# Optimization experiments

Measured on AMD Instinct MI355X. Metric: run time of the kernel, lower is better.

## Reference

```python
import jax, jax.numpy as jnp
import numpy as np

B, N, E = 16, 1000, 16000        # graphs, nodes/graph, edges/graph
H1, C1 = 8, 128                  # conv1 heads, per-head channels (hidden_size)
EMB, HID = 64, 128               # embed_size, mlp hidden_size


def gat_conv(x, ei, W, att_src, att_dst, bias, heads, concat):
    """PyG GATConv (eval mode, self-loops already in ei). x: [Ntot, Fin]."""
    Ntot = x.shape[0]
    C = W.shape[1] // heads
    h = (x @ W).reshape(Ntot, heads, C)                  # [Ntot, H, C]
    a_src = jnp.einsum('nhc,hc->nh', h, att_src)          # [Ntot, H]
    a_dst = jnp.einsum('nhc,hc->nh', h, att_dst)
    src, dst = ei[0], ei[1]
    alpha = jax.nn.leaky_relu(a_src[src] + a_dst[dst], 0.2)   # [Etot, H]
    # segment softmax over destination nodes (every node has a self loop)
    amax = jax.ops.segment_max(alpha, dst, num_segments=Ntot)
    ea = jnp.exp(alpha - amax[dst])
    denom = jax.ops.segment_sum(ea, dst, num_segments=Ntot)
    alpha = ea / denom[dst]
    msg = h[src] * alpha[:, :, None]                      # [Etot, H, C]
    out = jax.ops.segment_sum(msg, dst, num_segments=Ntot)   # [Ntot, H, C]
    out = out.reshape(Ntot, heads * C) if concat else out.mean(axis=1)
    return out + bias


def setup_inputs():
    key = jax.random.key(0)
    k = jax.random.split(key, 16)
    g = lambda kk, sh: (jax.random.normal(kk, sh, jnp.float32) * 0.1)
    return {
        'actions': jax.random.normal(k[0], (B, N, 2), jnp.float32),
        'node_features': jax.random.normal(k[1], (B, 1, N), jnp.float32),
        'edge_index': jax.random.randint(k[2], (B, 2, E), 0, N, dtype=jnp.int32),
        # conv1: GATConv(3, C1, heads=H1, concat=True)
        'W1': g(k[3], (3, H1 * C1)),
        'att_src1': g(k[4], (H1, C1)),
        'att_dst1': g(k[5], (H1, C1)),
        'b1': g(k[6], (H1 * C1,)),
        # conv2: GATConv(H1*C1, EMB, heads=1, concat=False)
        'W2': g(k[7], (H1 * C1, EMB)),
        'att_src2': g(k[8], (1, EMB)),
        'att_dst2': g(k[9], (1, EMB)),
        'b2': g(k[10], (EMB,)),
        # MLP head
        'mlp_w1': g(k[11], (N * EMB, HID)),
        'mlp_b1': jnp.zeros((HID,), jnp.float32),
        'mlp_w2': g(k[12], (HID, HID)),
        'mlp_b2': jnp.zeros((HID,), jnp.float32),
        'out_w': g(k[13], (HID, N)),
        'out_b': jnp.zeros((N,), jnp.float32),
    }


def reference(actions, node_features, edge_index, W1, att_src1, att_dst1, b1,
              W2, att_src2, att_dst2, b2, mlp_w1, mlp_b1, mlp_w2, mlp_b2,
              out_w, out_b):
    Bn, _, Nn = node_features.shape
    nf = node_features.astype(jnp.float32).squeeze(1)                 # [B, N]
    x = jnp.stack([actions[:, :, 0], actions[:, :, 1], nf], axis=2)   # [B, N, 3]
    x = x.reshape(Bn * Nn, 3)
    # batch-offset edge index, then faithful row-major reshape to [2, B*E]
    ei = (edge_index + (jnp.arange(Bn) * Nn)[:, None, None]).reshape(2, -1)
    loops = jnp.broadcast_to(jnp.arange(Bn * Nn)[None, :], (2, Bn * Nn))
    ei = jnp.concatenate([ei, loops], axis=1)
    # eval mode: dropouts are no-ops
    x = jax.nn.elu(gat_conv(x, ei, W1, att_src1, att_dst1, b1, H1, True))
    x = jax.nn.elu(gat_conv(x, ei, W2, att_src2, att_dst2, b2, 1, False))
    x = x.reshape(Bn, Nn * EMB)
    x = jax.nn.relu(x @ mlp_w1 + mlp_b1)
    x = jax.nn.relu(x @ mlp_w2 + mlp_b2)
    return jax.nn.sigmoid(x @ out_w + out_b)                          # [B, N]
```

## Files before the change

### kernel.cpp

```cpp
#include <hip/hip_runtime.h>
#include <math.h>

#define NB 16
#define NN 1000
#define NT 16000
#define NE 16000
#define EBASE 256000
#define ETOT 272000
#define F1 1024
#define EMB 64
#define HID 128
#define KTOT 64000
#define MLP1B 1024
#define NREP 8
#define CAP 96

typedef unsigned short ushort_t;
typedef unsigned int uint_t;
typedef __attribute__((ext_vector_type(8))) _Float16 half8;
typedef __attribute__((ext_vector_type(4))) float float4_;
typedef __attribute__((ext_vector_type(2))) float float2_;
typedef __attribute__((ext_vector_type(2))) uint_t uint2_;

__device__ __forceinline__ int src_of(const int* ei, int j) {
    if (j < EBASE) return ei[j] + (j / 32000) * 1000;
    return j - EBASE;
}
__device__ __forceinline__ int dst_of(const int* ei, int j) {
    if (j < EBASE) return ei[EBASE + j] + (8 + j / 32000) * 1000;
    return j - EBASE;
}

__device__ __forceinline__ float lrelu02(float r) { return r >= 0.f ? r : 0.2f * r; }
__device__ __forceinline__ float elu1(float v)    { return v > 0.f ? v : expm1f(v); }
__device__ __forceinline__ ushort_t f2h(float f) {
    _Float16 h = (_Float16)f;
    union { _Float16 h; ushort_t u; } c; c.h = h; return c.u;
}

__global__ __launch_bounds__(1024) void k_prep0(
    const float* __restrict__ actions, const float* __restrict__ nf,
    const float* __restrict__ W1, const float* __restrict__ as1w, const float* __restrict__ ad1w,
    const float* __restrict__ W2,
    float* __restrict__ x4, float* __restrict__ as1, float* __restrict__ ad1,
    ushort_t* __restrict__ w2f, int* __restrict__ cnt, float* __restrict__ y1rep) {
    __shared__ float tile[64][65];
    __shared__ float was[24], wad[24];
    int bid = blockIdx.x, t = threadIdx.x;

    int zi = bid * 1024 + t;
    if (zi < NT) cnt[zi] = 0;
    if (bid >= 16) y1rep[(size_t)(bid - 16) * 1024 + t] = 0.f;

    if (bid < 16) {
        if (t < 24) {
            int k = t / 8, h = t % 8;
            float ss = 0.f, dd = 0.f;
            for (int c = 0; c < 128; ++c) {
                float w = W1[k * F1 + h * 128 + c];
                ss += w * as1w[h * 128 + c];
                dd += w * ad1w[h * 128 + c];
            }
            was[t] = ss; wad[t] = dd;
        }
        __syncthreads();
        int n = bid * 1000 + t;
        if (t < 1000) {
            float x0 = actions[n * 2 + 0];
            float x1v = actions[n * 2 + 1];
            float x2v = nf[n];
            float4_ xv = {x0, x1v, x2v, 0.f};
            *(float4_*)(x4 + (size_t)n * 4) = xv;
            #pragma unroll
            for (int h = 0; h < 8; ++h) {
                as1[n * 8 + h] = x0 * was[h] + x1v * was[8 + h] + x2v * was[16 + h];
                ad1[n * 8 + h] = x0 * wad[h] + x1v * wad[8 + h] + x2v * wad[16 + h];
            }
        }
    } else {
        int k0 = (bid - 16) * 64;
        int c = t & 63, g = t >> 6;
        for (int r = g; r < 64; r += 16)
            tile[r][c] = W2[(size_t)(k0 + r) * 64 + c];
        __syncthreads();
        if (t < 512) {
            int q = t;
            int t4 = q >> 7, ksl = (q >> 6) & 1, l8 = q & 63;
            int kg = l8 >> 4, mrow = l8 & 15;
            int n = t4 * 16 + mrow;
            int kloc = ksl * 32 + kg * 8;
            size_t base = (((size_t)t4 * 32 + (k0 >> 5) + ksl) * 64 + l8) * 8;
            #pragma unroll
            for (int j = 0; j < 8; ++j)
                w2f[base + j] = f2h(tile[kloc + j][n]);
        }
    }
}

__global__ void k_fillslots(const int* __restrict__ ei, int* __restrict__ cnt,
                            int* __restrict__ esrc) {
    int j = blockIdx.x * blockDim.x + threadIdx.x;
    if (j >= ETOT) return;
    int dv = dst_of(ei, j);
    int slot = atomicAdd(&cnt[dv], 1);
    if (slot < CAP) esrc[(size_t)dv * CAP + slot] = src_of(ei, j);
}

__global__ __launch_bounds__(256) void k_conv1h2(
    const int* __restrict__ cnt, const int* __restrict__ esrc, const float* __restrict__ x4,
    const float* __restrict__ as1, const float* __restrict__ ad1,
    const float* __restrict__ W1, const float* __restrict__ b1,
    const ushort_t* __restrict__ w2f,
    const float* __restrict__ as2w, const float* __restrict__ ad2w,
    float* __restrict__ h2, float* __restrict__ a2s, float* __restrict__ a2d) {
    __shared__ ushort_t x1t[16][1032];
    __shared__ float smb[16][8][3];
    __shared__ float a2p[4][16][2];
    int t = threadIdx.x, wave = t >> 6, lane = t & 63;

    float4_ w0 = *(const float4_*)(W1 + t * 4);
    float4_ w1r = *(const float4_*)(W1 + F1 + t * 4);
    float4_ w2r = *(const float4_*)(W1 + 2 * F1 + t * 4);
    float4_ bb = *(const float4_*)(b1 + t * 4);

    int g = lane >> 4, lg = lane & 15, eslot = lg >> 3, h = lg & 7;
    int nd0 = wave * 4 + g;
    int d = blockIdx.x * 16 + nd0;
    int cn = cnt[d];
    const int* ep = esrc + (size_t)d * CAP;
    float adv = ad1[d * 8 + h];
    float den = 0.f, s0 = 0.f, s1 = 0.f, s2 = 0.f;
    for (int e = eslot; e < cn; e += 2) {
        int s = ep[e];
        float ea = __expf(lrelu02(as1[s * 8 + h] + adv));
        float4_ xv = *(const float4_*)(x4 + (size_t)s * 4);
        den += ea; s0 += ea * xv.x; s1 += ea * xv.y; s2 += ea * xv.z;
    }
    den += __shfl_xor(den, 8, 64);
    s0  += __shfl_xor(s0, 8, 64);
    s1  += __shfl_xor(s1, 8, 64);
    s2  += __shfl_xor(s2, 8, 64);
    if (eslot == 0) {
        float inv = 1.f / den;
        smb[nd0][h][0] = s0 * inv;
        smb[nd0][h][1] = s1 * inv;
        smb[nd0][h][2] = s2 * inv;
    }
    __syncthreads();

    int hh = t >> 5;
    #pragma unroll 4
    for (int nd = 0; nd < 16; ++nd) {
        float c0 = smb[nd][hh][0], c1 = smb[nd][hh][1], c2 = smb[nd][hh][2];
        float v0 = c0 * w0.x + c1 * w1r.x + c2 * w2r.x + bb.x;
        float v1 = c0 * w0.y + c1 * w1r.y + c2 * w2r.y + bb.y;
        float v2 = c0 * w0.z + c1 * w1r.z + c2 * w2r.z + bb.z;
        float v3 = c0 * w0.w + c1 * w1r.w + c2 * w2r.w + bb.w;
        v0 = elu1(v0); v1 = elu1(v1); v2 = elu1(v2); v3 = elu1(v3);
        uint2_ pk;
        pk.x = (uint_t)f2h(v0) | ((uint_t)f2h(v1) << 16);
        pk.y = (uint_t)f2h(v2) | ((uint_t)f2h(v3) << 16);
        *(uint2_*)(&x1t[nd][t * 4]) = pk;
    }
    __syncthreads();

    int mrow = lane & 15, kg = lane >> 4;
    const ushort_t* bp = w2f + ((size_t)wave * 32 * 64 + lane) * 8;
    float4_ acc = {0.f, 0.f, 0.f, 0.f};
    #pragma unroll 8
    for (int ks = 0; ks < 32; ++ks) {
        half8 a = *(const half8*)(&x1t[mrow][kg * 8 + ks * 32]);
        half8 b = *(const half8*)(bp + (size_t)ks * 512);
        acc = __builtin_amdgcn_mfma_f32_16x16x32_f16(a, b, acc, 0, 0, 0);
    }
    int row0 = blockIdx.x * 16;
    #pragma unroll
    for (int r = 0; r < 4; ++r)
        h2[(size_t)(row0 + kg * 4 + r) * EMB + wave * 16 + mrow] = acc[r];

    float sw = as2w[wave * 16 + mrow], dw = ad2w[wave * 16 + mrow];
    float ps[4], pd[4];
    #pragma unroll
    for (int r = 0; r < 4; ++r) { ps[r] = acc[r] * sw; pd[r] = acc[r] * dw; }
    #pragma unroll
    for (int st = 1; st < 16; st <<= 1) {
        #pragma unroll
        for (int r = 0; r < 4; ++r) {
            ps[r] += __shfl_xor(ps[r], st, 64);
            pd[r] += __shfl_xor(pd[r], st, 64);
        }
    }
    if (mrow == 0) {
        #pragma unroll
        for (int r = 0; r < 4; ++r) {
            a2p[wave][kg * 4 + r][0] = ps[r];
            a2p[wave][kg * 4 + r][1] = pd[r];
        }
    }
    __syncthreads();
    if (t < 16) {
        float ss = a2p[0][t][0] + a2p[1][t][0] + a2p[2][t][0] + a2p[3][t][0];
        float dd = a2p[0][t][1] + a2p[1][t][1] + a2p[2][t][1] + a2p[3][t][1];
        a2s[row0 + t] = ss; a2d[row0 + t] = dd;
    }
}

__global__ __launch_bounds__(256) void k_conv2(
    const int* __restrict__ cnt, const int* __restrict__ esrc, const float* __restrict__ h2,
    const float* __restrict__ a2s, const float* __restrict__ a2d, const float* __restrict__ b2,
    float* __restrict__ x2) {
    int t = threadIdx.x;
    int wave = t >> 6, lane = t & 63;
    int d = blockIdx.x * 4 + wave;
    int cn = cnt[d];
    const int* ep = esrc + (size_t)d * CAP;
    float adv = a2d[d];
    int eg = lane >> 4, c4 = (lane & 15) * 4;

    float den = 0.f;
    float4_ acc = {0.f, 0.f, 0.f, 0.f};
    for (int e = eg; e < cn; e += 4) {
        int s = ep[e];
        float ea = __expf(lrelu02(a2s[s] + adv));
        float4_ hv = *(const float4_*)(h2 + (size_t)s * EMB + c4);
        den += ea;
        acc.x += ea * hv.x; acc.y += ea * hv.y; acc.z += ea * hv.z; acc.w += ea * hv.w;
    }
    #pragma unroll
    for (int st = 16; st < 64; st <<= 1) {
        den   += __shfl_xor(den, st, 64);
        acc.x += __shfl_xor(acc.x, st, 64);
        acc.y += __shfl_xor(acc.y, st, 64);
        acc.z += __shfl_xor(acc.z, st, 64);
        acc.w += __shfl_xor(acc.w, st, 64);
    }
    if (eg == 0) {
        float inv = 1.f / den;
        float4_ o;
        o.x = elu1(acc.x * inv + b2[c4 + 0]);
        o.y = elu1(acc.y * inv + b2[c4 + 1]);
        o.z = elu1(acc.z * inv + b2[c4 + 2]);
        o.w = elu1(acc.w * inv + b2[c4 + 3]);
        *(float4_*)(x2 + (size_t)d * EMB + c4) = o;
    }
}

__global__ __launch_bounds__(256) void k_mlp1(const float* __restrict__ x2,
                                              const float* __restrict__ w1,
                                              float* __restrict__ y1rep) {
    __shared__ float red[NB * HID];
    int t = threadIdx.x;
    int wave = t >> 6, lane = t & 63;
    int j2 = lane * 2;
    float2_ acc[NB];
    #pragma unroll
    for (int b = 0; b < NB; ++b) acc[b] = (float2_){0.f, 0.f};

    for (int k = blockIdx.x * 4 + wave; k < KTOT; k += MLP1B * 4) {
        int kk = __builtin_amdgcn_readfirstlane(k);
        float2_ w = *(const float2_*)(w1 + (size_t)kk * HID + j2);
        const float* xr = x2 + kk;
        #pragma unroll
        for (int b = 0; b < NB; ++b) {
            float xv = xr[(size_t)b * KTOT];
            acc[b].x += xv * w.x;
            acc[b].y += xv * w.y;
        }
    }
    for (int w = 0; w < 4; ++w) {
        if (wave == w) {
            #pragma unroll
            for (int b = 0; b < NB; ++b) {
                if (w == 0) {
                    red[b * HID + j2]     = acc[b].x;
                    red[b * HID + j2 + 1] = acc[b].y;
                } else {
                    red[b * HID + j2]     += acc[b].x;
                    red[b * HID + j2 + 1] += acc[b].y;
                }
            }
        }
        __syncthreads();
    }
    float* yp = y1rep + (size_t)(blockIdx.x & (NREP - 1)) * (NB * HID);
    for (int idx = t; idx < NB * HID; idx += 256)
        atomicAdd(&yp[idx], red[idx]);
}

__global__ __launch_bounds__(256) void k_tail(
    const float* __restrict__ y1rep, const float* __restrict__ mb1,
    const float* __restrict__ mw2, const float* __restrict__ mb2,
    const float* __restrict__ ow, const float* __restrict__ ob,
    float* __restrict__ out) {
    __shared__ float y1[NB * HID];
    __shared__ float y2s[NB * HID];
    __shared__ float oacc[16][16][17];
    int t = threadIdx.x;

    for (int idx = t; idx < NB * HID; idx += 256) {
        float s = 0.f;
        #pragma unroll
        for (int r = 0; r < NREP; ++r)
            s += y1rep[(size_t)r * (NB * HID) + idx];
        y1[idx] = fmaxf(s + mb1[idx & 127], 0.f);
    }
    __syncthreads();

    #pragma unroll
    for (int i = 0; i < 8; ++i) {
        int o = t + i * 256;
        int b = o >> 7, j = o & 127;
        float acc = mb2[j];
        for (int k = 0; k < HID; ++k) acc += y1[b * HID + k] * mw2[k * HID + j];
        y2s[o] = fmaxf(acc, 0.f);
    }
    __syncthreads();

    int nl = t & 15, jg = t >> 4;
    int n = blockIdx.x * 16 + nl;
    float acc[NB];
    #pragma unroll
    for (int b = 0; b < NB; ++b) acc[b] = 0.f;
    if (n < NN) {
        #pragma unroll
        for (int jj = 0; jj < 8; ++jj) {
            int j = jg * 8 + jj;
            float w = ow[j * NN + n];
            #pragma unroll
            for (int b = 0; b < NB; ++b) acc[b] += y2s[b * HID + j] * w;
        }
    }
    #pragma unroll
    for (int b = 0; b < NB; ++b) oacc[jg][nl][b] = acc[b];
    __syncthreads();
    int b = t >> 4, nl2 = t & 15;
    float s = 0.f;
    #pragma unroll
    for (int q = 0; q < 16; ++q) s += oacc[q][nl2][b];
    int n2 = blockIdx.x * 16 + nl2;
    if (n2 < NN)
        out[b * NN + n2] = 1.f / (1.f + __expf(-(s + ob[n2])));
}

extern "C" void kernel_launch(void* const* d_in, const int* in_sizes, int n_in,
                              void* d_out, int out_size, void* d_ws, size_t ws_size,
                              hipStream_t stream) {
    const float* actions = (const float*)d_in[0];
    const float* nf      = (const float*)d_in[1];
    const int*   ei      = (const int*)d_in[2];
    const float* W1      = (const float*)d_in[3];
    const float* as1w    = (const float*)d_in[4];
    const float* ad1w    = (const float*)d_in[5];
    const float* b1      = (const float*)d_in[6];
    const float* W2      = (const float*)d_in[7];
    const float* as2w    = (const float*)d_in[8];
    const float* ad2w    = (const float*)d_in[9];
    const float* b2      = (const float*)d_in[10];
    const float* mw1     = (const float*)d_in[11];
    const float* mb1     = (const float*)d_in[12];
    const float* mw2     = (const float*)d_in[13];
    const float* mb2     = (const float*)d_in[14];
    const float* ow      = (const float*)d_in[15];
    const float* ob      = (const float*)d_in[16];
    float* out = (float*)d_out;

    float* f = (float*)d_ws;
    float* x4    = f;  f += (size_t)NT * 4;
    float* h2    = f;  f += (size_t)NT * EMB;
    float* x2    = f;  f += (size_t)NT * EMB;
    float* as1   = f;  f += NT * 8;
    float* ad1   = f;  f += NT * 8;
    float* a2s   = f;  f += NT;
    float* a2d   = f;  f += NT;
    float* y1rep = f;  f += (size_t)NREP * NB * HID;
    ushort_t* w2f = (ushort_t*)f;
    int* ip = (int*)(w2f + 65536);
    int* cnt  = ip; ip += NT;
    int* esrc = ip; ip += (size_t)NT * CAP;

    k_prep0<<<32, 1024, 0, stream>>>(actions, nf, W1, as1w, ad1w, W2, x4, as1, ad1, w2f, cnt, y1rep);
    k_fillslots<<<(ETOT + 255) / 256, 256, 0, stream>>>(ei, cnt, esrc);
    k_conv1h2<<<NT / 16, 256, 0, stream>>>(cnt, esrc, x4, as1, ad1, W1, b1, w2f,
                                           as2w, ad2w, h2, a2s, a2d);
    k_conv2<<<NT / 4, 256, 0, stream>>>(cnt, esrc, h2, a2s, a2d, b2, x2);
    k_mlp1<<<MLP1B, 256, 0, stream>>>(x2, mw1, y1rep);
    k_tail<<<64, 256, 0, stream>>>(y1rep, mb1, mw2, mb2, ow, ob, out);
}
```

Baseline: 204.2 us.

## Merge prep with edge slot filling and fuse MLP tail via grid-wide counter

Combines the prep kernel and the edge-bucketing kernel into one launch with 256-thread blocks, and replaces the in-kernel zeroing with a single memset of the counters, accumulators and a done flag. The MLP first-layer kernel and the tail kernel are fused. The first 64 blocks spin on an atomic completion counter until all 1024 blocks have added their partials, then run the tail. This removes kernel launch gaps. The cost is an extra memset, plus a spin-wait that relies on all 1024 blocks being co-resident or scheduled ahead of the waiting blocks; launch_bounds(256,4) is set to support that.

```diff
diff --git a/kernel.cpp b/kernel.cpp
--- a/kernel.cpp
+++ b/kernel.cpp
@@ -38,21 +38,17 @@
     union { _Float16 h; ushort_t u; } c; c.h = h; return c.u;
 }
 
-__global__ __launch_bounds__(1024) void k_prep0(
+__global__ __launch_bounds__(256) void k_prepfill(
     const float* __restrict__ actions, const float* __restrict__ nf,
     const float* __restrict__ W1, const float* __restrict__ as1w, const float* __restrict__ ad1w,
-    const float* __restrict__ W2,
+    const float* __restrict__ W2, const int* __restrict__ ei,
     float* __restrict__ x4, float* __restrict__ as1, float* __restrict__ ad1,
-    ushort_t* __restrict__ w2f, int* __restrict__ cnt, float* __restrict__ y1rep) {
+    ushort_t* __restrict__ w2f, int* __restrict__ cnt, int* __restrict__ esrc) {
     __shared__ float tile[64][65];
     __shared__ float was[24], wad[24];
     int bid = blockIdx.x, t = threadIdx.x;
 
-    int zi = bid * 1024 + t;
-    if (zi < NT) cnt[zi] = 0;
-    if (bid >= 16) y1rep[(size_t)(bid - 16) * 1024 + t] = 0.f;
-
-    if (bid < 16) {
+    if (bid < 63) {
         if (t < 24) {
             int k = t / 8, h = t % 8;
             float ss = 0.f, dd = 0.f;
@@ -64,8 +60,8 @@
             was[t] = ss; wad[t] = dd;
         }
         __syncthreads();
-        int n = bid * 1000 + t;
-        if (t < 1000) {
+        int n = bid * 256 + t;
+        if (n < NT) {
             float x0 = actions[n * 2 + 0];
             float x1v = actions[n * 2 + 1];
             float x2v = nf[n];
@@ -77,14 +73,13 @@
                 ad1[n * 8 + h] = x0 * wad[h] + x1v * wad[8 + h] + x2v * wad[16 + h];
             }
         }
-    } else {
-        int k0 = (bid - 16) * 64;
+    } else if (bid < 79) {
+        int k0 = (bid - 63) * 64;
         int c = t & 63, g = t >> 6;
-        for (int r = g; r < 64; r += 16)
+        for (int r = g; r < 64; r += 4)
             tile[r][c] = W2[(size_t)(k0 + r) * 64 + c];
         __syncthreads();
-        if (t < 512) {
-            int q = t;
+        for (int q = t; q < 512; q += 256) {
             int t4 = q >> 7, ksl = (q >> 6) & 1, l8 = q & 63;
             int kg = l8 >> 4, mrow = l8 & 15;
             int n = t4 * 16 + mrow;
@@ -94,16 +89,14 @@
             for (int j = 0; j < 8; ++j)
                 w2f[base + j] = f2h(tile[kloc + j][n]);
         }
-    }
-}
-
-__global__ void k_fillslots(const int* __restrict__ ei, int* __restrict__ cnt,
-                            int* __restrict__ esrc) {
-    int j = blockIdx.x * blockDim.x + threadIdx.x;
-    if (j >= ETOT) return;
-    int dv = dst_of(ei, j);
-    int slot = atomicAdd(&cnt[dv], 1);
-    if (slot < CAP) esrc[(size_t)dv * CAP + slot] = src_of(ei, j);
+    } else {
+        int j = (bid - 79) * 256 + t;
+        if (j < ETOT) {
+            int dv = dst_of(ei, j);
+            int slot = atomicAdd(&cnt[dv], 1);
+            if (slot < CAP) esrc[(size_t)dv * CAP + slot] = src_of(ei, j);
+        }
+    }
 }
 
 __global__ __launch_bounds__(256) void k_conv1h2(
@@ -245,10 +238,20 @@
     }
 }
 
-__global__ __launch_bounds__(256) void k_mlp1(const float* __restrict__ x2,
-                                              const float* __restrict__ w1,
-                                              float* __restrict__ y1rep) {
-    __shared__ float red[NB * HID];
+__global__ __launch_bounds__(256, 4) void k_mlp1tail(
+    const float* __restrict__ x2, const float* __restrict__ w1,
+    float* __restrict__ y1rep, int* __restrict__ done,
+    const float* __restrict__ mb1, const float* __restrict__ mw2,
+    const float* __restrict__ mb2, const float* __restrict__ ow,
+    const float* __restrict__ ob, float* __restrict__ out) {
+    __shared__ union {
+        float red[NB * HID];
+        struct {
+            float y1[NB * HID];
+            float y2s[NB * HID];
+            float oacc[16][16][17];
+        } tl;
+    } sm;
     int t = threadIdx.x;
     int wave = t >> 6, lane = t & 63;
     int j2 = lane * 2;
@@ -272,11 +275,11 @@
             #pragma unroll
             for (int b = 0; b < NB; ++b) {
                 if (w == 0) {
-                    red[b * HID + j2]     = acc[b].x;
-                    red[b * HID + j2 + 1] = acc[b].y;
+                    sm.red[b * HID + j2]     = acc[b].x;
+                    sm.red[b * HID + j2 + 1] = acc[b].y;
                 } else {
-                    red[b * HID + j2]     += acc[b].x;
-                    red[b * HID + j2 + 1] += acc[b].y;
+                    sm.red[b * HID + j2]     += acc[b].x;
+                    sm.red[b * HID + j2 + 1] += acc[b].y;
                 }
             }
         }
@@ -284,25 +287,25 @@
     }
     float* yp = y1rep + (size_t)(blockIdx.x & (NREP - 1)) * (NB * HID);
     for (int idx = t; idx < NB * HID; idx += 256)
-        atomicAdd(&yp[idx], red[idx]);
-}
-
-__global__ __launch_bounds__(256) void k_tail(
-    const float* __restrict__ y1rep, const float* __restrict__ mb1,
-    const float* __restrict__ mw2, const float* __restrict__ mb2,
-    const float* __restrict__ ow, const float* __restrict__ ob,
-    float* __restrict__ out) {
-    __shared__ float y1[NB * HID];
-    __shared__ float y2s[NB * HID];
-    __shared__ float oacc[16][16][17];
-    int t = threadIdx.x;
+        atomicAdd(&yp[idx], sm.red[idx]);
+
+    __threadfence();
+    __syncthreads();
+    if (t == 0)
+        __hip_atomic_fetch_add(done, 1, __ATOMIC_ACQ_REL, __HIP_MEMORY_SCOPE_AGENT);
+    if (blockIdx.x >= 64) return;
+
+    if (t == 0) {
+        while (__hip_atomic_load(done, __ATOMIC_ACQUIRE, __HIP_MEMORY_SCOPE_AGENT) < MLP1B) { }
+    }
+    __syncthreads();
 
     for (int idx = t; idx < NB * HID; idx += 256) {
         float s = 0.f;
         #pragma unroll
         for (int r = 0; r < NREP; ++r)
             s += y1rep[(size_t)r * (NB * HID) + idx];
-        y1[idx] = fmaxf(s + mb1[idx & 127], 0.f);
+        sm.tl.y1[idx] = fmaxf(s + mb1[idx & 127], 0.f);
     }
     __syncthreads();
 
@@ -310,33 +313,33 @@
     for (int i = 0; i < 8; ++i) {
         int o = t + i * 256;
         int b = o >> 7, j = o & 127;
-        float acc = mb2[j];
-        for (int k = 0; k < HID; ++k) acc += y1[b * HID + k] * mw2[k * HID + j];
-        y2s[o] = fmaxf(acc, 0.f);
+        float a = mb2[j];
+        for (int k = 0; k < HID; ++k) a += sm.tl.y1[b * HID + k] * mw2[k * HID + j];
+        sm.tl.y2s[o] = fmaxf(a, 0.f);
     }
     __syncthreads();
 
     int nl = t & 15, jg = t >> 4;
     int n = blockIdx.x * 16 + nl;
-    float acc[NB];
-    #pragma unroll
-    for (int b = 0; b < NB; ++b) acc[b] = 0.f;
+    float oa[NB];
+    #pragma unroll
+    for (int b = 0; b < NB; ++b) oa[b] = 0.f;
     if (n < NN) {
         #pragma unroll
         for (int jj = 0; jj < 8; ++jj) {
             int j = jg * 8 + jj;
             float w = ow[j * NN + n];
             #pragma unroll
-            for (int b = 0; b < NB; ++b) acc[b] += y2s[b * HID + j] * w;
-        }
-    }
-    #pragma unroll
-    for (int b = 0; b < NB; ++b) oacc[jg][nl][b] = acc[b];
+            for (int b = 0; b < NB; ++b) oa[b] += sm.tl.y2s[b * HID + j] * w;
+        }
+    }
+    #pragma unroll
+    for (int b = 0; b < NB; ++b) sm.tl.oacc[jg][nl][b] = oa[b];
     __syncthreads();
     int b = t >> 4, nl2 = t & 15;
     float s = 0.f;
     #pragma unroll
-    for (int q = 0; q < 16; ++q) s += oacc[q][nl2][b];
+    for (int q = 0; q < 16; ++q) s += sm.tl.oacc[q][nl2][b];
     int n2 = blockIdx.x * 16 + nl2;
     if (n2 < NN)
         out[b * NN + n2] = 1.f / (1.f + __expf(-(s + ob[n2])));
@@ -372,17 +375,20 @@
     float* ad1   = f;  f += NT * 8;
     float* a2s   = f;  f += NT;
     float* a2d   = f;  f += NT;
-    float* y1rep = f;  f += (size_t)NREP * NB * HID;
     ushort_t* w2f = (ushort_t*)f;
     int* ip = (int*)(w2f + 65536);
-    int* cnt  = ip; ip += NT;
-    int* esrc = ip; ip += (size_t)NT * CAP;
-
-    k_prep0<<<32, 1024, 0, stream>>>(actions, nf, W1, as1w, ad1w, W2, x4, as1, ad1, w2f, cnt, y1rep);
-    k_fillslots<<<(ETOT + 255) / 256, 256, 0, stream>>>(ei, cnt, esrc);
+    int* cnt     = ip;            ip += NT;
+    float* y1rep = (float*)ip;    ip += NREP * NB * HID;
+    int* done    = ip;            ip += 4;
+    int* esrc    = ip;            ip += (size_t)NT * CAP;
+
+    hipMemsetAsync(cnt, 0, (size_t)(NT + NREP * NB * HID + 4) * sizeof(int), stream);
+
+    k_prepfill<<<1142, 256, 0, stream>>>(actions, nf, W1, as1w, ad1w, W2, ei,
+                                         x4, as1, ad1, w2f, cnt, esrc);
     k_conv1h2<<<NT / 16, 256, 0, stream>>>(cnt, esrc, x4, as1, ad1, W1, b1, w2f,
                                            as2w, ad2w, h2, a2s, a2d);
     k_conv2<<<NT / 4, 256, 0, stream>>>(cnt, esrc, h2, a2s, a2d, b2, x2);
-    k_mlp1<<<MLP1B, 256, 0, stream>>>(x2, mw1, y1rep);
-    k_tail<<<64, 256, 0, stream>>>(y1rep, mb1, mw2, mb2, ow, ob, out);
-}
+    k_mlp1tail<<<MLP1B, 256, 0, stream>>>(x2, mw1, y1rep, done,
+                                          mb1, mw2, mb2, ow, ob, out);
+}
```

Result: slower. 317.1 us (+55.3%).
